# Optimization experiments

Measured on AMD Instinct MI355X. Metric: run time of the kernel, lower is better.

Reference implementation:

```python
import jax, jax.numpy as jnp
import numpy as np

N_NODES = 10000
N_EDGES = 160000
HIDDEN = 512
N_LAYERS = 5


def setup_inputs() -> dict:
    key = jax.random.key(0)
    ks = jax.random.split(key, 12)
    return {
        "feat": jax.random.normal(ks[0], (N_NODES, HIDDEN), dtype=jnp.float32),
        "adj_row": jax.random.randint(ks[1], (N_EDGES,), 0, N_NODES, dtype=jnp.int32),
        "adj_col": jax.random.randint(ks[2], (N_EDGES,), 0, N_NODES, dtype=jnp.int32),
        "adj_val": jax.random.uniform(ks[3], (N_EDGES,), dtype=jnp.float32),
        "Wg": jax.random.normal(ks[4], (N_LAYERS, HIDDEN, HIDDEN), dtype=jnp.float32) * 0.02,
        "bg": jnp.zeros((N_LAYERS, HIDDEN), dtype=jnp.float32),
        "vw1": jax.random.normal(ks[5], (HIDDEN, HIDDEN), dtype=jnp.float32) * 0.02,
        "vb1": jnp.zeros((HIDDEN,), dtype=jnp.float32),
        "vw2": jax.random.normal(ks[6], (HIDDEN, 1), dtype=jnp.float32) * 0.02,
        "vb2": jnp.zeros((1,), dtype=jnp.float32),
    }


def _spmm(adj_row, adj_col, adj_val, x, n):
    # out[r] = sum_e adj_val[e] * x[adj_col[e]] for edges with adj_row[e] == r
    gathered = adj_val[:, None] * x[adj_col]  # [E, H]
    return jax.ops.segment_sum(gathered, adj_row, num_segments=n)


def reference(feat, adj_row, adj_col, adj_val, Wg, bg, vw1, vb1, vw2, vb2):
    n = feat.shape[0]
    x = feat
    for i in range(N_LAYERS):  # 5 structurally identical GraphConv layers
        h = x @ Wg[i]                                 # dense GEMM [N,H]
        agg = _spmm(adj_row, adj_col, adj_val, h, n)  # sparse aggregation
        x = jax.nn.relu(agg + bg[i])                  # bias + ReLU (dropout = eval identity)
    h = jax.nn.relu(x @ vw1 + vb1)
    return jax.nn.sigmoid(h @ vw2 + vb2)  # [N, 1]
```

## Files before the change

### kernel.cpp

```cpp
#include <hip/hip_runtime.h>

#define H 512
#define NNODES 10000
#define NEDGES 160000
#define NLAYERS 5
#define TM 160
#define NMT 63
#define HISTB 625

typedef __attribute__((ext_vector_type(8))) short short8;
typedef __attribute__((ext_vector_type(4))) float floatx4;

__device__ inline unsigned short f2bf(float v) {
    union { float f; unsigned int u; } x; x.f = v;
    unsigned int r = (x.u + 0x7fffu + ((x.u >> 16) & 1u)) >> 16;
    return (unsigned short)r;
}
__device__ inline float bf2f(unsigned short u) {
    union { unsigned int u; float f; } x; x.u = ((unsigned int)u) << 16; return x.f;
}
__device__ inline void gl_lds16(const void* g, void* l) {
    __builtin_amdgcn_global_load_lds((const __attribute__((address_space(1))) void*)g,
                                     (__attribute__((address_space(3))) void*)l, 16, 0, 0);
}

#define PB_ZERO1 79
#define PB_ZERO2 1875
#define PB_CVT   5000
#define PB_WF    192
__global__ __launch_bounds__(256)
void fused_prep(int* __restrict__ counts, int* __restrict__ ev,
                const float* __restrict__ feat, unsigned short* __restrict__ x,
                const float* __restrict__ Wg, const float* __restrict__ vw1,
                unsigned short* __restrict__ Wfrag) {
    const int b = blockIdx.x;
    const int t = threadIdx.x;
    if (b < PB_ZERO1) {
        int i = b * 256 + t;
        if (i < 20000) counts[i] = 0;
    } else if (b < PB_ZERO1 + PB_ZERO2) {
        int i = (b - PB_ZERO1) * 256 + t;
        if (i < 480000) ev[i] = 0;
    } else if (b < PB_ZERO1 + PB_ZERO2 + PB_CVT) {
        int i = (b - PB_ZERO1 - PB_ZERO2) * 256 + t;
        if (i < NNODES * H / 4) {
            float4 v = ((const float4*)feat)[i];
            ushort4 o;
            o.x = f2bf(v.x); o.y = f2bf(v.y); o.z = f2bf(v.z); o.w = f2bf(v.w);
            ((ushort4*)x)[i] = o;
        }
    } else {
        const int bb = b - PB_ZERO1 - PB_ZERO2 - PB_CVT;
        const int z = bb >> 5;
        const int rem = bb & 31;
        const float* in = (z < NLAYERS) ? (Wg + (size_t)z * H * H) : vw1;
        unsigned short* outp = Wfrag + ((size_t)(z * 32 + rem) * 8192);
        const int colbase = rem * 16;
#pragma unroll
        for (int q = 0; q < 4; ++q) {
            const int p = t + 256 * q;
            const int ks = p >> 6, lane = p & 63;
            const int col = colbase + (lane & 15);
            const int kb = ks * 32 + (lane >> 4) * 8;
            short8 o;
#pragma unroll
            for (int e = 0; e < 8; ++e)
                o[e] = (short)f2bf(in[(size_t)(kb + e) * H + col]);
            *(short8*)(outp + (size_t)p * 8) = o;
        }
    }
}

__global__ __launch_bounds__(1024)
void scan_rows_pad(const int* __restrict__ counts, int* __restrict__ row_ptr, int n) {
    __shared__ int sums[1024];
    const int t = threadIdx.x;
    const int base = t * 16;
    int local[16];
    int s = 0;
#pragma unroll
    for (int i = 0; i < 16; ++i) {
        int idx = base + i;
        int v = (idx < n) ? ((counts[idx] + 7) & ~7) : 0;
        local[i] = s;
        s += v;
    }
    sums[t] = s;
    __syncthreads();
    for (int off = 1; off < 1024; off <<= 1) {
        int v = (t >= off) ? sums[t - off] : 0;
        __syncthreads();
        sums[t] += v;
        __syncthreads();
    }
    const int prefix = (t == 0) ? 0 : sums[t - 1];
#pragma unroll
    for (int i = 0; i < 16; ++i) {
        int idx = base + i;
        if (idx < n) row_ptr[idx] = prefix + local[i];
    }
    if (t == 0) row_ptr[n] = sums[1023];
}

__global__ void edge_scatter(const int* __restrict__ rows, const int* __restrict__ colsin,
                             const float* __restrict__ valsin, const int* __restrict__ row_ptr,
                             int* __restrict__ fill, int2* __restrict__ ev, int n) {
    int i = blockIdx.x * blockDim.x + threadIdx.x;
    if (i < n) {
        int r = rows[i];
        int pos = row_ptr[r] + atomicAdd(&fill[r], 1);
        int2 e; e.x = colsin[i]; e.y = __float_as_int(valsin[i]);
        ev[pos] = e;
    }
}

__global__ __launch_bounds__(256)
void gemm_bf16_160f(const unsigned short* __restrict__ A, const unsigned short* __restrict__ WfragZ,
                    unsigned short* __restrict__ C, const float* __restrict__ bias,
                    int has_bias_relu, int M,
                    const int* __restrict__ hrows, int* __restrict__ hcounts) {
    if (blockIdx.x >= 512) {
        const int i = (blockIdx.x - 512) * 256 + threadIdx.x;
        if (i < NEDGES) atomicAdd(&hcounts[hrows[i]], 1);
        return;
    }
    __shared__ __align__(16) unsigned short lsA[TM * 64];
    const int L = blockIdx.x;
    const int ml = L & 7;
    const int rest = L >> 3;
    const int n = rest & 7;
    const int mh = rest >> 3;
    const int m = mh * 8 + ml;
    if (m >= NMT) return;
    const int tileM = m * TM;
    const int tileN = n * 64;

    const int t = threadIdx.x;
    const int lane = t & 63;
    const int wave = t >> 6;
    const int wm = wave >> 1, wn = wave & 1;
    const int quad = lane >> 4, r16 = lane & 15;

    floatx4 acc[5][2] = {};

    const unsigned short* ap[5];
#pragma unroll
    for (int q = 0; q < 5; ++q) {
        const int c = t + 256 * q;
        const int row = c >> 3;
        int g = tileM + row; if (g >= M) g = M - 1;
        ap[q] = A + (size_t)g * 512 + (((c & 7) ^ (row & 7)) * 8);
    }
    const unsigned short* bbase[2];
#pragma unroll
    for (int j = 0; j < 2; ++j)
        bbase[j] = WfragZ + ((size_t)(n * 4 + wn * 2 + j) * 16) * 512 + lane * 8;

    for (int it = 0; it < 8; ++it) {
        const int k0 = it * 64;
#pragma unroll
        for (int q = 0; q < 5; ++q)
            gl_lds16(ap[q] + k0, lsA + (size_t)(t + 256 * q) * 8);
        short8 bfr[2][2];
#pragma unroll
        for (int j = 0; j < 2; ++j)
#pragma unroll
            for (int kk = 0; kk < 2; ++kk)
                bfr[j][kk] = *(const short8*)(bbase[j] + (size_t)(it * 2 + kk) * 512);
        __syncthreads();

        short8 af[5][2];
#pragma unroll
        for (int i = 0; i < 5; ++i) {
            const int row = wm * 80 + i * 16 + r16;
#pragma unroll
            for (int kk = 0; kk < 2; ++kk) {
                const int kcw = kk * 4 + quad;
                af[i][kk] = *(const short8*)&lsA[(size_t)(row * 8 + (kcw ^ (row & 7))) * 8];
            }
        }
#pragma unroll
        for (int kk = 0; kk < 2; ++kk)
#pragma unroll
            for (int i = 0; i < 5; ++i)
#pragma unroll
                for (int j = 0; j < 2; ++j)
                    acc[i][j] = __builtin_amdgcn_mfma_f32_16x16x32_bf16(af[i][kk], bfr[j][kk], acc[i][j], 0, 0, 0);
        __syncthreads();
    }

#pragma unroll
    for (int i = 0; i < 5; ++i) {
#pragma unroll
        for (int j = 0; j < 2; ++j) {
            const int col = tileN + wn * 32 + j * 16 + r16;
#pragma unroll
            for (int reg = 0; reg < 4; ++reg) {
                const int row = tileM + wm * 80 + i * 16 + quad * 4 + reg;
                if (row < M) {
                    float v = acc[i][j][reg];
                    if (has_bias_relu) { v += bias[col]; v = fmaxf(v, 0.f); }
                    C[(size_t)row * 512 + col] = f2bf(v);
                }
            }
        }
    }
}

__global__ __launch_bounds__(256)
void spmm_pad(const int* __restrict__ prow, const int2* __restrict__ ev,
              const unsigned short* __restrict__ hmat,
              const float* __restrict__ bias, unsigned short* __restrict__ xout) {
    const int wave = threadIdx.x >> 6, lane = threadIdx.x & 63;
    const int r = blockIdx.x * 4 + wave;
    if (r >= NNODES) return;
    const int s = prow[r], e = prow[r + 1];
    const int cb = lane * 8;
    float acc[8] = {0.f, 0.f, 0.f, 0.f, 0.f, 0.f, 0.f, 0.f};

    for (int i = s; i < e; i += 8) {
        int2 cv[8]; short8 g[8];
#pragma unroll
        for (int u = 0; u < 8; ++u) cv[u] = ev[i + u];
#pragma unroll
        for (int u = 0; u < 8; ++u) g[u] = *(const short8*)(hmat + (size_t)cv[u].x * H + cb);
#pragma unroll
        for (int u = 0; u < 8; ++u) {
            const float v = __int_as_float(cv[u].y);
#pragma unroll
            for (int j = 0; j < 8; ++j) acc[j] += v * bf2f((unsigned short)g[u][j]);
        }
    }

    short8 o;
#pragma unroll
    for (int j = 0; j < 8; ++j)
        o[j] = (short)f2bf(fmaxf(acc[j] + bias[cb + j], 0.f));
    *(short8*)(xout + (size_t)r * H + cb) = o;
}

__global__ __launch_bounds__(256)
void final_head(const unsigned short* __restrict__ h2, const float* __restrict__ w2,
                const float* __restrict__ b2, float* __restrict__ out, int n) {
    const int wave = threadIdx.x >> 6, lane = threadIdx.x & 63;
    const int r = blockIdx.x * 4 + wave;
    if (r >= n) return;
    const unsigned short* hrow = h2 + (size_t)r * H;
    float acc = 0.f;
#pragma unroll
    for (int i = 0; i < 8; ++i) {
        const int c = lane * 8 + i;
        acc += bf2f(hrow[c]) * w2[c];
    }
#pragma unroll
    for (int off = 32; off >= 1; off >>= 1) acc += __shfl_xor(acc, off, 64);
    if (lane == 0) out[r] = 1.f / (1.f + expf(-(acc + b2[0])));
}

extern "C" void kernel_launch(void* const* d_in, const int* in_sizes, int n_in,
                              void* d_out, int out_size, void* d_ws, size_t ws_size,
                              hipStream_t stream) {
    (void)in_sizes; (void)n_in; (void)out_size; (void)ws_size;
    const float* feat   = (const float*)d_in[0];
    const int* adj_row  = (const int*)d_in[1];
    const int* adj_col  = (const int*)d_in[2];
    const float* adj_val= (const float*)d_in[3];
    const float* Wg     = (const float*)d_in[4];
    const float* bg     = (const float*)d_in[5];
    const float* vw1    = (const float*)d_in[6];
    const float* vb1    = (const float*)d_in[7];
    const float* vw2    = (const float*)d_in[8];
    const float* vb2    = (const float*)d_in[9];
    float* out = (float*)d_out;

    char* ws = (char*)d_ws;
    unsigned short* x     = (unsigned short*)(ws + 0);
    unsigned short* h     = (unsigned short*)(ws + 10240000);
    unsigned short* Wfrag = (unsigned short*)(ws + 20480000);
    int*   prow    = (int*)(ws + 23625728);
    int*   counts  = (int*)(ws + 23785792);
    int*   fill    = (int*)(ws + 23825792);
    int*   ev      = (int*)(ws + 23865792);

    fused_prep<<<PB_ZERO1 + PB_ZERO2 + PB_CVT + PB_WF, 256, 0, stream>>>(
        counts, ev, feat, x, Wg, vw1, Wfrag);

    gemm_bf16_160f<<<512 + HISTB, 256, 0, stream>>>(x, Wfrag, h, nullptr, 0, NNODES,
                                                    adj_row, counts);
    scan_rows_pad<<<1, 1024, 0, stream>>>(counts, prow, NNODES);
    edge_scatter<<<(NEDGES + 255) / 256, 256, 0, stream>>>(adj_row, adj_col, adj_val,
                                                           prow, fill, (int2*)ev, NEDGES);
    spmm_pad<<<(NNODES + 3) / 4, 256, 0, stream>>>(prow, (const int2*)ev, h, bg, x);

    for (int l = 1; l < NLAYERS; ++l) {
        gemm_bf16_160f<<<512, 256, 0, stream>>>(x, Wfrag + (size_t)l * H * H, h, nullptr, 0,
                                                NNODES, adj_row, counts);
        spmm_pad<<<(NNODES + 3) / 4, 256, 0, stream>>>(prow, (const int2*)ev, h,
                                                       bg + (size_t)l * H, x);
    }
    gemm_bf16_160f<<<512, 256, 0, stream>>>(x, Wfrag + (size_t)NLAYERS * H * H, h, vb1, 1,
                                            NNODES, adj_row, counts);
    final_head<<<(NNODES + 3) / 4, 256, 0, stream>>>(h, vw2, vb2, out, NNODES);
}
```

Before: 332.9 us.

## Store activations in MFMA fragment layout and load GEMM operands directly

The activation matrix x is now written by the prep conversion and by spmm in a pre-swizzled MFMA fragment order. The GEMM can then load A fragments straight from global memory into registers, dropping the LDS staging buffer and both block barriers. This removes shared-memory traffic and synchronisation in the GEMM. The cost is that A rows are no longer shared through LDS across the two N-waves, so global/L2 reads of A double, and spmm output stores become scattered 16-byte writes.

```diff
diff --git a/kernel.cpp b/kernel.cpp
--- a/kernel.cpp
+++ b/kernel.cpp
@@ -19,14 +19,11 @@
 __device__ inline float bf2f(unsigned short u) {
     union { unsigned int u; float f; } x; x.u = ((unsigned int)u) << 16; return x.f;
 }
-__device__ inline void gl_lds16(const void* g, void* l) {
-    __builtin_amdgcn_global_load_lds((const __attribute__((address_space(1))) void*)g,
-                                     (__attribute__((address_space(3))) void*)l, 16, 0, 0);
-}
+
 
 #define PB_ZERO1 79
 #define PB_ZERO2 1875
-#define PB_CVT   5000
+#define PB_CVT   2500
 #define PB_WF    192
 __global__ __launch_bounds__(256)
 void fused_prep(int* __restrict__ counts, int* __restrict__ ev,
@@ -43,12 +40,17 @@
         if (i < 480000) ev[i] = 0;
     } else if (b < PB_ZERO1 + PB_ZERO2 + PB_CVT) {
         int i = (b - PB_ZERO1 - PB_ZERO2) * 256 + t;
-        if (i < NNODES * H / 4) {
-            float4 v = ((const float4*)feat)[i];
-            ushort4 o;
-            o.x = f2bf(v.x); o.y = f2bf(v.y); o.z = f2bf(v.z); o.w = f2bf(v.w);
-            ((ushort4*)x)[i] = o;
-        }
+        const int row = i >> 6, chunk = i & 63;
+        const float* src = feat + (size_t)row * 512 + chunk * 8;
+        float4 v0 = ((const float4*)src)[0];
+        float4 v1 = ((const float4*)src)[1];
+        short8 o;
+        o[0] = (short)f2bf(v0.x); o[1] = (short)f2bf(v0.y);
+        o[2] = (short)f2bf(v0.z); o[3] = (short)f2bf(v0.w);
+        o[4] = (short)f2bf(v1.x); o[5] = (short)f2bf(v1.y);
+        o[6] = (short)f2bf(v1.z); o[7] = (short)f2bf(v1.w);
+        const size_t g = (size_t)(row >> 4) * 1024 + (chunk >> 2) * 64 + (chunk & 3) * 16 + (row & 15);
+        *(short8*)(x + g * 8) = o;
     } else {
         const int bb = b - PB_ZERO1 - PB_ZERO2 - PB_CVT;
         const int z = bb >> 5;
@@ -115,16 +117,15 @@
 }
 
 __global__ __launch_bounds__(256)
-void gemm_bf16_160f(const unsigned short* __restrict__ A, const unsigned short* __restrict__ WfragZ,
-                    unsigned short* __restrict__ C, const float* __restrict__ bias,
-                    int has_bias_relu, int M,
-                    const int* __restrict__ hrows, int* __restrict__ hcounts) {
+void gemm_ff(const unsigned short* __restrict__ A, const unsigned short* __restrict__ Wz,
+             unsigned short* __restrict__ C, const float* __restrict__ bias,
+             int has_bias_relu,
+             const int* __restrict__ hrows, int* __restrict__ hcounts) {
     if (blockIdx.x >= 512) {
         const int i = (blockIdx.x - 512) * 256 + threadIdx.x;
         if (i < NEDGES) atomicAdd(&hcounts[hrows[i]], 1);
         return;
     }
-    __shared__ __align__(16) unsigned short lsA[TM * 64];
     const int L = blockIdx.x;
     const int ml = L & 7;
     const int rest = L >> 3;
@@ -143,41 +144,29 @@
 
     floatx4 acc[5][2] = {};
 
-    const unsigned short* ap[5];
-#pragma unroll
-    for (int q = 0; q < 5; ++q) {
-        const int c = t + 256 * q;
-        const int row = c >> 3;
-        int g = tileM + row; if (g >= M) g = M - 1;
-        ap[q] = A + (size_t)g * 512 + (((c & 7) ^ (row & 7)) * 8);
-    }
-    const unsigned short* bbase[2];
+    const unsigned short* ab[5];
+#pragma unroll
+    for (int i = 0; i < 5; ++i) {
+        int rg = m * 10 + wm * 5 + i;
+        if (rg > 624) rg = 624;
+        ab[i] = A + (size_t)rg * 8192 + lane * 8;
+    }
+    const unsigned short* bb[2];
 #pragma unroll
     for (int j = 0; j < 2; ++j)
-        bbase[j] = WfragZ + ((size_t)(n * 4 + wn * 2 + j) * 16) * 512 + lane * 8;
+        bb[j] = Wz + ((size_t)(n * 4 + wn * 2 + j) * 16) * 512 + lane * 8;
 
     for (int it = 0; it < 8; ++it) {
-        const int k0 = it * 64;
-#pragma unroll
-        for (int q = 0; q < 5; ++q)
-            gl_lds16(ap[q] + k0, lsA + (size_t)(t + 256 * q) * 8);
-        short8 bfr[2][2];
-#pragma unroll
-        for (int j = 0; j < 2; ++j)
-#pragma unroll
-            for (int kk = 0; kk < 2; ++kk)
-                bfr[j][kk] = *(const short8*)(bbase[j] + (size_t)(it * 2 + kk) * 512);
-        __syncthreads();
-
-        short8 af[5][2];
-#pragma unroll
-        for (int i = 0; i < 5; ++i) {
-            const int row = wm * 80 + i * 16 + r16;
-#pragma unroll
-            for (int kk = 0; kk < 2; ++kk) {
-                const int kcw = kk * 4 + quad;
-                af[i][kk] = *(const short8*)&lsA[(size_t)(row * 8 + (kcw ^ (row & 7))) * 8];
-            }
+        short8 af[5][2], bf[2][2];
+#pragma unroll
+        for (int kk = 0; kk < 2; ++kk) {
+            const int ks = it * 2 + kk;
+#pragma unroll
+            for (int i = 0; i < 5; ++i)
+                af[i][kk] = *(const short8*)(ab[i] + (size_t)ks * 512);
+#pragma unroll
+            for (int j = 0; j < 2; ++j)
+                bf[j][kk] = *(const short8*)(bb[j] + (size_t)ks * 512);
         }
 #pragma unroll
         for (int kk = 0; kk < 2; ++kk)
@@ -185,8 +174,7 @@
             for (int i = 0; i < 5; ++i)
 #pragma unroll
                 for (int j = 0; j < 2; ++j)
-                    acc[i][j] = __builtin_amdgcn_mfma_f32_16x16x32_bf16(af[i][kk], bfr[j][kk], acc[i][j], 0, 0, 0);
-        __syncthreads();
+                    acc[i][j] = __builtin_amdgcn_mfma_f32_16x16x32_bf16(af[i][kk], bf[j][kk], acc[i][j], 0, 0, 0);
     }
 
 #pragma unroll
@@ -197,7 +185,7 @@
 #pragma unroll
             for (int reg = 0; reg < 4; ++reg) {
                 const int row = tileM + wm * 80 + i * 16 + quad * 4 + reg;
-                if (row < M) {
+                if (row < NNODES) {
                     float v = acc[i][j][reg];
                     if (has_bias_relu) { v += bias[col]; v = fmaxf(v, 0.f); }
                     C[(size_t)row * 512 + col] = f2bf(v);
@@ -236,7 +224,8 @@
 #pragma unroll
     for (int j = 0; j < 8; ++j)
         o[j] = (short)f2bf(fmaxf(acc[j] + bias[cb + j], 0.f));
-    *(short8*)(xout + (size_t)r * H + cb) = o;
+    const size_t g = (size_t)(r >> 4) * 1024 + (lane >> 2) * 64 + (lane & 3) * 16 + (r & 15);
+    *(short8*)(xout + g * 8) = o;
 }
 
 __global__ __launch_bounds__(256)
@@ -285,20 +274,19 @@
     fused_prep<<<PB_ZERO1 + PB_ZERO2 + PB_CVT + PB_WF, 256, 0, stream>>>(
         counts, ev, feat, x, Wg, vw1, Wfrag);
 
-    gemm_bf16_160f<<<512 + HISTB, 256, 0, stream>>>(x, Wfrag, h, nullptr, 0, NNODES,
-                                                    adj_row, counts);
+    gemm_ff<<<512 + HISTB, 256, 0, stream>>>(x, Wfrag, h, nullptr, 0, adj_row, counts);
     scan_rows_pad<<<1, 1024, 0, stream>>>(counts, prow, NNODES);
     edge_scatter<<<(NEDGES + 255) / 256, 256, 0, stream>>>(adj_row, adj_col, adj_val,
                                                            prow, fill, (int2*)ev, NEDGES);
     spmm_pad<<<(NNODES + 3) / 4, 256, 0, stream>>>(prow, (const int2*)ev, h, bg, x);
 
     for (int l = 1; l < NLAYERS; ++l) {
-        gemm_bf16_160f<<<512, 256, 0, stream>>>(x, Wfrag + (size_t)l * H * H, h, nullptr, 0,
-                                                NNODES, adj_row, counts);
+        gemm_ff<<<512, 256, 0, stream>>>(x, Wfrag + (size_t)l * H * H, h, nullptr, 0,
+                                         adj_row, counts);
         spmm_pad<<<(NNODES + 3) / 4, 256, 0, stream>>>(prow, (const int2*)ev, h,
                                                        bg + (size_t)l * H, x);
     }
-    gemm_bf16_160f<<<512, 256, 0, stream>>>(x, Wfrag + (size_t)NLAYERS * H * H, h, vb1, 1,
-                                            NNODES, adj_row, counts);
+    gemm_ff<<<512, 256, 0, stream>>>(x, Wfrag + (size_t)NLAYERS * H * H, h, vb1, 1,
+                                     adj_row, counts);
     final_head<<<(NNODES + 3) / 4, 256, 0, stream>>>(h, vw2, vb2, out, NNODES);
 }
```

Result: slower. 410.1 us (+23.2%).
